# Performance work log

Measured on AMD Instinct MI355X. Metric: run time of the kernel, lower is better.

Reference implementation:

```python
import jax, jax.numpy as jnp
import numpy as np

LMDA = 1.0
SMOOTH = 1e-05

# 13 directional offsets (dz, dy, dx) matching the original slice pairs 1..13
OFFSETS = [
    (1, 0, 0), (0, 1, 0), (0, 0, 1),
    (1, 1, 0), (1, -1, 0),
    (0, 1, 1), (0, 1, -1),
    (1, 0, -1), (1, 0, 1),
    (1, -1, -1), (1, 1, -1),
    (-1, -1, -1), (-1, 1, -1),
]


def _shifted_diff(x, off):
    """x[..., pos-shift] - x[..., neg-shift] for offset off over last 3 dims."""
    sl_pos = tuple(slice(1, None) if o == 1 else (slice(None, -1) if o == -1 else slice(None)) for o in off)
    sl_neg = tuple(slice(None, -1) if o == 1 else (slice(1, None) if o == -1 else slice(None)) for o in off)
    return x[(Ellipsis,) + sl_pos] - x[(Ellipsis,) + sl_neg]


def setup_inputs() -> dict:
    key = jax.random.key(0)
    k1, k2 = jax.random.split(key)
    shape = (4, 1, 128, 192, 192)
    eps = 1e-6
    inp = jax.random.uniform(k1, shape, dtype=jnp.float32, minval=eps, maxval=1.0 - eps)
    tgt = jax.random.uniform(k2, shape, dtype=jnp.float32, minval=0.0, maxval=1.0)
    return {"input": inp, "target": tgt}


def reference(input, target):
    # region term: BCE with mean reduction
    bce = -jnp.mean(target * jnp.log(input) + (1.0 - target) * jnp.log(1.0 - input))

    # boundary term: 13 directional diff-product ratios
    acc = jnp.float32(0.0)
    for off in OFFSETS:
        di = _shifted_diff(input, off)
        dt = _shifted_diff(target, off)
        acc = acc + jnp.sum(di * dt) / (jnp.sum(dt * dt) + SMOOTH)
    boundary = 1.0 - acc / 13.0

    return LMDA * bce + boundary
```

## Files before the change

### kernel.cpp

```cpp
#include <hip/hip_runtime.h>
#include <math.h>

#define DX 192
#define DY 192
#define DZ 128
#define DB 4
#define DXY (DX*DY)
#define NTOT (DB*DZ*DXY)
#define NV (NTOT/4)
#define XV (DX/4)


__device__ inline float wred(float v) {
    #pragma unroll
    for (int o = 32; o > 0; o >>= 1) v += __shfl_down(v, o, 64);
    return v;
}

__global__ __launch_bounds__(256) void gc3d_main(const float* __restrict__ inp,
                                                 const float* __restrict__ tgt,
                                                 double* __restrict__ acc) {
    float s0=0,s1=0,s2=0,s3=0,s4=0,s5=0,s6=0,s7=0,s8=0,s9=0,s10=0,s11=0,s12=0;
    float r0=0,r1=0,r2=0,r3=0,r4=0,r5=0,r6=0,r7=0,r8=0,r9=0,r10=0,r11=0,r12=0;
    float bces = 0.f;

    int tid = blockIdx.x * blockDim.x + threadIdx.x;
    int stride = gridDim.x * blockDim.x;

    for (int v = tid; v < NV; v += stride) {
        int xv4 = v % XV;
        int rem = v / XV;
        int y = rem % DY;
        int z = (rem / DY) % DZ;
        int x0 = xv4 * 4;

        bool zv = (z != DZ - 1);
        bool yv = (y != DY - 1);
        int oz = zv ? DXY : 0;
        int oy = yv ? DX : 0;
        int xe = (x0 != DX - 4) ? 4 : 3;
        float fz = zv ? 1.f : 0.f;
        float fy = yv ? 1.f : 0.f;
        float fx3 = (x0 != DX - 4) ? 1.f : 0.f;

        long base = (long)v * 4;
        const float* ip = inp + base;
        const float* tp = tgt + base;

        float4 i00 = *(const float4*)(ip);
        float4 i01 = *(const float4*)(ip + oy);
        float4 i10 = *(const float4*)(ip + oz);
        float4 i11 = *(const float4*)(ip + oz + oy);
        float4 t00 = *(const float4*)(tp);
        float4 t01 = *(const float4*)(tp + oy);
        float4 t10 = *(const float4*)(tp + oz);
        float4 t11 = *(const float4*)(tp + oz + oy);
        float i00e = ip[xe],        i01e = ip[oy + xe];
        float i10e = ip[oz + xe],   i11e = ip[oz + oy + xe];
        float t00e = tp[xe],        t01e = tp[oy + xe];
        float t10e = tp[oz + xe],   t11e = tp[oz + oy + xe];

        #define PROC_ELEM(c0,c1,c2,c3,c4,c5,c6,c7, d0,d1,d2,d3,d4,d5,d6,d7, FX) do { \
            float fzy = fz*fy, fyx = fy*(FX), fzx = fz*(FX), fzyx = fzy*(FX); \
            float di, dt, dtm; \
            di=c4-c0; dt=d4-d0; dtm=fz  *dt; s0 +=di*dtm; r0 +=dt*dtm; \
            di=c2-c0; dt=d2-d0; dtm=fy  *dt; s1 +=di*dtm; r1 +=dt*dtm; \
            di=c1-c0; dt=d1-d0; dtm=(FX)*dt; s2 +=di*dtm; r2 +=dt*dtm; \
            di=c6-c0; dt=d6-d0; dtm=fzy *dt; s3 +=di*dtm; r3 +=dt*dtm; \
            di=c4-c2; dt=d4-d2; dtm=fzy *dt; s4 +=di*dtm; r4 +=dt*dtm; \
            di=c3-c0; dt=d3-d0; dtm=fyx *dt; s5 +=di*dtm; r5 +=dt*dtm; \
            di=c2-c1; dt=d2-d1; dtm=fyx *dt; s6 +=di*dtm; r6 +=dt*dtm; \
            di=c4-c1; dt=d4-d1; dtm=fzx *dt; s7 +=di*dtm; r7 +=dt*dtm; \
            di=c5-c0; dt=d5-d0; dtm=fzx *dt; s8 +=di*dtm; r8 +=dt*dtm; \
            di=c4-c3; dt=d4-d3; dtm=fzyx*dt; s9 +=di*dtm; r9 +=dt*dtm; \
            di=c6-c1; dt=d6-d1; dtm=fzyx*dt; s10+=di*dtm; r10+=dt*dtm; \
            di=c7-c0; dt=d7-d0; dtm=fzyx*dt; s11+=di*dtm; r11+=dt*dtm; \
            di=c5-c2; dt=d5-d2; dtm=fzyx*dt; s12+=di*dtm; r12+=dt*dtm; \
            bces += d0*__logf(c0) + (1.0f - d0)*__logf(1.0f - c0); \
        } while (0)

        PROC_ELEM(i00.x,i00.y,i01.x,i01.y,i10.x,i10.y,i11.x,i11.y,
                  t00.x,t00.y,t01.x,t01.y,t10.x,t10.y,t11.x,t11.y, 1.0f);
        PROC_ELEM(i00.y,i00.z,i01.y,i01.z,i10.y,i10.z,i11.y,i11.z,
                  t00.y,t00.z,t01.y,t01.z,t10.y,t10.z,t11.y,t11.z, 1.0f);
        PROC_ELEM(i00.z,i00.w,i01.z,i01.w,i10.z,i10.w,i11.z,i11.w,
                  t00.z,t00.w,t01.z,t01.w,t10.z,t10.w,t11.z,t11.w, 1.0f);
        PROC_ELEM(i00.w,i00e, i01.w,i01e, i10.w,i10e, i11.w,i11e,
                  t00.w,t00e, t01.w,t01e, t10.w,t10e, t11.w,t11e, fx3);
        #undef PROC_ELEM
    }

    float vals[27] = {s0,s1,s2,s3,s4,s5,s6,s7,s8,s9,s10,s11,s12,
                      r0,r1,r2,r3,r4,r5,r6,r7,r8,r9,r10,r11,r12, bces};
    #pragma unroll
    for (int k = 0; k < 27; k++) vals[k] = wred(vals[k]);

    __shared__ float red[4][27];
    int lane = threadIdx.x & 63;
    int wave = threadIdx.x >> 6;
    if (lane == 0) {
        #pragma unroll
        for (int k = 0; k < 27; k++) red[wave][k] = vals[k];
    }
    __syncthreads();
    if (threadIdx.x < 27) {
        float t = red[0][threadIdx.x] + red[1][threadIdx.x]
                + red[2][threadIdx.x] + red[3][threadIdx.x];
        atomicAdd(&acc[threadIdx.x], (double)t);
    }
}

__global__ void gc3d_final(const double* __restrict__ acc, float* __restrict__ out) {
    if (threadIdx.x == 0 && blockIdx.x == 0) {
        double s = 0.0;
        #pragma unroll
        for (int k = 0; k < 13; k++) s += acc[k] / (acc[13 + k] + 1e-5);
        double bce = -acc[26] / (double)NTOT;
        out[0] = (float)(bce + 1.0 - s / 13.0);
    }
}

extern "C" void kernel_launch(void* const* d_in, const int* in_sizes, int n_in,
                              void* d_out, int out_size, void* d_ws, size_t ws_size,
                              hipStream_t stream) {
    const float* inp = (const float*)d_in[0];
    const float* tgt = (const float*)d_in[1];
    double* acc = (double*)d_ws;

    hipMemsetAsync(d_ws, 0, 27 * sizeof(double), stream);
    gc3d_main<<<1536, 256, 0, stream>>>(inp, tgt, acc);
    gc3d_final<<<1, 64, 0, stream>>>(acc, (float*)d_out);
}
```

Measured before the change: 224.0 us.

## Tile 8-wide x strips over z-chunks with register reuse and interior specialization

Each thread now handles an 8-element x strip across a 4-slice z chunk, keeping the upper z-plane rows in registers as the next lower plane instead of reloading them. This cuts redundant global and cache loads, since the old version read four rows per four elements. An INTERIOR template drops the boundary mask multiplies for threads away from the z and y edges, and the BCE term is rewritten to use one fewer multiply. The grid is sized exactly to the work, with no grid-stride loop. In exchange each thread holds more registers, there are far more blocks, and each block still issues its own atomics.

```diff
diff --git a/kernel.cpp b/kernel.cpp
--- a/kernel.cpp
+++ b/kernel.cpp
@@ -6,101 +6,133 @@
 #define DZ 128
 #define DB 4
 #define DXY (DX*DY)
-#define NTOT (DB*DZ*DXY)
-#define NV (NTOT/4)
-#define XV (DX/4)
+#define XG 24
+#define ZC 4
+#define NCK (DZ/ZC)
+#define NBLK (DB*NCK*DY*XG/256)
 
 
-__device__ inline float wred(float v) {
+struct Acc { float s[13]; float r[13]; float bce; };
+
+__device__ inline void load9(float (&a)[9], const float* __restrict__ p, int xe) {
+    float4 u = *(const float4*)(p);
+    float4 v = *(const float4*)(p + 4);
+    a[0]=u.x; a[1]=u.y; a[2]=u.z; a[3]=u.w;
+    a[4]=v.x; a[5]=v.y; a[6]=v.z; a[7]=v.w;
+    a[8] = p[xe];
+}
+
+template<bool INTERIOR>
+__device__ inline void compute8(const float (&Ia)[9], const float (&Ib)[9],
+                                const float (&Ja)[9], const float (&Jb)[9],
+                                const float (&Ta)[9], const float (&Tb)[9],
+                                const float (&Ua)[9], const float (&Ub)[9],
+                                float fz, float fy, float fx7, Acc& A)
+{
     #pragma unroll
-    for (int o = 32; o > 0; o >>= 1) v += __shfl_down(v, o, 64);
-    return v;
+    for (int e = 0; e < 8; ++e) {
+        const float fx = (e < 7) ? 1.0f : fx7;
+        float mzy, myx, mzx, mzyx;
+        if (INTERIOR) { mzy = 1.0f; myx = fx; mzx = fx; mzyx = fx; }
+        else { mzy = fz*fy; myx = fy*fx; mzx = fz*fx; mzyx = mzy*fx; }
+        const float c0=Ia[e], c1=Ia[e+1], c2=Ib[e], c3=Ib[e+1];
+        const float c4=Ja[e], c5=Ja[e+1], c6=Jb[e], c7=Jb[e+1];
+        const float d0=Ta[e], d1=Ta[e+1], d2=Tb[e], d3=Tb[e+1];
+        const float d4=Ua[e], d5=Ua[e+1], d6=Ub[e], d7=Ub[e+1];
+        float di, dt, dtm;
+        di=c4-c0; dt=d4-d0;              A.s[0] +=di*dt;  A.r[0] +=dt*dt;
+        di=c2-c0; dt=d2-d0;              A.s[1] +=di*dt;  A.r[1] +=dt*dt;
+        di=c1-c0; dt=d1-d0;              A.s[2] +=di*dt;  A.r[2] +=dt*dt;
+        di=c6-c0; dt=d6-d0; dtm=mzy*dt;  A.s[3] +=di*dtm; A.r[3] +=dt*dtm;
+        di=c4-c2; dt=d4-d2; dtm=mzy*dt;  A.s[4] +=di*dtm; A.r[4] +=dt*dtm;
+        di=c3-c0; dt=d3-d0; dtm=myx*dt;  A.s[5] +=di*dtm; A.r[5] +=dt*dtm;
+        di=c2-c1; dt=d2-d1; dtm=myx*dt;  A.s[6] +=di*dtm; A.r[6] +=dt*dtm;
+        di=c4-c1; dt=d4-d1; dtm=mzx*dt;  A.s[7] +=di*dtm; A.r[7] +=dt*dtm;
+        di=c5-c0; dt=d5-d0; dtm=mzx*dt;  A.s[8] +=di*dtm; A.r[8] +=dt*dtm;
+        di=c4-c3; dt=d4-d3; dtm=mzyx*dt; A.s[9] +=di*dtm; A.r[9] +=dt*dtm;
+        di=c6-c1; dt=d6-d1; dtm=mzyx*dt; A.s[10]+=di*dtm; A.r[10]+=dt*dtm;
+        di=c7-c0; dt=d7-d0; dtm=mzyx*dt; A.s[11]+=di*dtm; A.r[11]+=dt*dtm;
+        di=c5-c2; dt=d5-d2; dtm=mzyx*dt; A.s[12]+=di*dtm; A.r[12]+=dt*dtm;
+        float l0 = __logf(c0), l1 = __logf(1.0f - c0);
+        A.bce += l1 + d0 * (l0 - l1);
+    }
+}
+
+template<bool INTERIOR>
+__device__ inline void zloop(const float* __restrict__ ip, const float* __restrict__ tp,
+                             int oy, int xe, float fy, float fx7, int z0, Acc& A)
+{
+    float Ia[9], Ib[9], Ta[9], Tb[9];
+    float Ja[9], Jb[9], Ua[9], Ub[9];
+    load9(Ia, ip, xe); load9(Ib, ip + oy, xe);
+    load9(Ta, tp, xe); load9(Tb, tp + oy, xe);
+    #pragma unroll 1
+    for (int k = 0; k < ZC/2; ++k) {
+        int z = z0 + 2*k;
+        {
+            int   oz = (INTERIOR || z < DZ-1) ? DXY : 0;
+            float fz = (INTERIOR || z < DZ-1) ? 1.0f : 0.0f;
+            load9(Ja, ip + oz, xe); load9(Jb, ip + oz + oy, xe);
+            load9(Ua, tp + oz, xe); load9(Ub, tp + oz + oy, xe);
+            compute8<INTERIOR>(Ia, Ib, Ja, Jb, Ta, Tb, Ua, Ub, fz, fy, fx7, A);
+            ip += DXY; tp += DXY;
+        }
+        {
+            int z1 = z + 1;
+            int   oz = (INTERIOR || z1 < DZ-1) ? DXY : 0;
+            float fz = (INTERIOR || z1 < DZ-1) ? 1.0f : 0.0f;
+            load9(Ia, ip + oz, xe); load9(Ib, ip + oz + oy, xe);
+            load9(Ta, tp + oz, xe); load9(Tb, tp + oz + oy, xe);
+            compute8<INTERIOR>(Ja, Jb, Ia, Ib, Ua, Ub, Ta, Tb, fz, fy, fx7, A);
+            ip += DXY; tp += DXY;
+        }
+    }
 }
 
 __global__ __launch_bounds__(256) void gc3d_main(const float* __restrict__ inp,
                                                  const float* __restrict__ tgt,
-                                                 double* __restrict__ acc) {
-    float s0=0,s1=0,s2=0,s3=0,s4=0,s5=0,s6=0,s7=0,s8=0,s9=0,s10=0,s11=0,s12=0;
-    float r0=0,r1=0,r2=0,r3=0,r4=0,r5=0,r6=0,r7=0,r8=0,r9=0,r10=0,r11=0,r12=0;
-    float bces = 0.f;
+                                                 double* __restrict__ acc)
+{
+    int gid = blockIdx.x * 256 + threadIdx.x;
+    int xg = gid % XG;
+    int t1 = gid / XG;
+    int y  = t1 % DY;
+    int t2 = t1 / DY;
+    int ck = t2 % NCK;
+    int b  = t2 / NCK;
+    int z0 = ck * ZC;
 
-    int tid = blockIdx.x * blockDim.x + threadIdx.x;
-    int stride = gridDim.x * blockDim.x;
+    long base = (((long)b * DZ + z0) * DY + y) * DX + xg * 8;
+    const float* ip = inp + base;
+    const float* tp = tgt + base;
+    int   oy  = (y < DY-1) ? DX : 0;
+    float fy  = (y < DY-1) ? 1.0f : 0.0f;
+    int   xe  = (xg < XG-1) ? 8 : 7;
+    float fx7 = (xg < XG-1) ? 1.0f : 0.0f;
 
-    for (int v = tid; v < NV; v += stride) {
-        int xv4 = v % XV;
-        int rem = v / XV;
-        int y = rem % DY;
-        int z = (rem / DY) % DZ;
-        int x0 = xv4 * 4;
+    Acc A;
+    #pragma unroll
+    for (int k = 0; k < 13; ++k) { A.s[k] = 0.f; A.r[k] = 0.f; }
+    A.bce = 0.f;
 
-        bool zv = (z != DZ - 1);
-        bool yv = (y != DY - 1);
-        int oz = zv ? DXY : 0;
-        int oy = yv ? DX : 0;
-        int xe = (x0 != DX - 4) ? 4 : 3;
-        float fz = zv ? 1.f : 0.f;
-        float fy = yv ? 1.f : 0.f;
-        float fx3 = (x0 != DX - 4) ? 1.f : 0.f;
+    if ((y < DY-1) && (ck < NCK-1)) zloop<true >(ip, tp, oy, xe, fy, fx7, z0, A);
+    else                            zloop<false>(ip, tp, oy, xe, fy, fx7, z0, A);
 
-        long base = (long)v * 4;
-        const float* ip = inp + base;
-        const float* tp = tgt + base;
-
-        float4 i00 = *(const float4*)(ip);
-        float4 i01 = *(const float4*)(ip + oy);
-        float4 i10 = *(const float4*)(ip + oz);
-        float4 i11 = *(const float4*)(ip + oz + oy);
-        float4 t00 = *(const float4*)(tp);
-        float4 t01 = *(const float4*)(tp + oy);
-        float4 t10 = *(const float4*)(tp + oz);
-        float4 t11 = *(const float4*)(tp + oz + oy);
-        float i00e = ip[xe],        i01e = ip[oy + xe];
-        float i10e = ip[oz + xe],   i11e = ip[oz + oy + xe];
-        float t00e = tp[xe],        t01e = tp[oy + xe];
-        float t10e = tp[oz + xe],   t11e = tp[oz + oy + xe];
-
-        #define PROC_ELEM(c0,c1,c2,c3,c4,c5,c6,c7, d0,d1,d2,d3,d4,d5,d6,d7, FX) do { \
-            float fzy = fz*fy, fyx = fy*(FX), fzx = fz*(FX), fzyx = fzy*(FX); \
-            float di, dt, dtm; \
-            di=c4-c0; dt=d4-d0; dtm=fz  *dt; s0 +=di*dtm; r0 +=dt*dtm; \
-            di=c2-c0; dt=d2-d0; dtm=fy  *dt; s1 +=di*dtm; r1 +=dt*dtm; \
-            di=c1-c0; dt=d1-d0; dtm=(FX)*dt; s2 +=di*dtm; r2 +=dt*dtm; \
-            di=c6-c0; dt=d6-d0; dtm=fzy *dt; s3 +=di*dtm; r3 +=dt*dtm; \
-            di=c4-c2; dt=d4-d2; dtm=fzy *dt; s4 +=di*dtm; r4 +=dt*dtm; \
-            di=c3-c0; dt=d3-d0; dtm=fyx *dt; s5 +=di*dtm; r5 +=dt*dtm; \
-            di=c2-c1; dt=d2-d1; dtm=fyx *dt; s6 +=di*dtm; r6 +=dt*dtm; \
-            di=c4-c1; dt=d4-d1; dtm=fzx *dt; s7 +=di*dtm; r7 +=dt*dtm; \
-            di=c5-c0; dt=d5-d0; dtm=fzx *dt; s8 +=di*dtm; r8 +=dt*dtm; \
-            di=c4-c3; dt=d4-d3; dtm=fzyx*dt; s9 +=di*dtm; r9 +=dt*dtm; \
-            di=c6-c1; dt=d6-d1; dtm=fzyx*dt; s10+=di*dtm; r10+=dt*dtm; \
-            di=c7-c0; dt=d7-d0; dtm=fzyx*dt; s11+=di*dtm; r11+=dt*dtm; \
-            di=c5-c2; dt=d5-d2; dtm=fzyx*dt; s12+=di*dtm; r12+=dt*dtm; \
-            bces += d0*__logf(c0) + (1.0f - d0)*__logf(1.0f - c0); \
-        } while (0)
-
-        PROC_ELEM(i00.x,i00.y,i01.x,i01.y,i10.x,i10.y,i11.x,i11.y,
-                  t00.x,t00.y,t01.x,t01.y,t10.x,t10.y,t11.x,t11.y, 1.0f);
-        PROC_ELEM(i00.y,i00.z,i01.y,i01.z,i10.y,i10.z,i11.y,i11.z,
-                  t00.y,t00.z,t01.y,t01.z,t10.y,t10.z,t11.y,t11.z, 1.0f);
-        PROC_ELEM(i00.z,i00.w,i01.z,i01.w,i10.z,i10.w,i11.z,i11.w,
-                  t00.z,t00.w,t01.z,t01.w,t10.z,t10.w,t11.z,t11.w, 1.0f);
-        PROC_ELEM(i00.w,i00e, i01.w,i01e, i10.w,i10e, i11.w,i11e,
-                  t00.w,t00e, t01.w,t01e, t10.w,t10e, t11.w,t11e, fx3);
-        #undef PROC_ELEM
+    float vals[27];
+    #pragma unroll
+    for (int k = 0; k < 13; ++k) { vals[k] = A.s[k]; vals[13+k] = A.r[k]; }
+    vals[26] = A.bce;
+    #pragma unroll
+    for (int k = 0; k < 27; ++k) {
+        #pragma unroll
+        for (int o = 32; o > 0; o >>= 1) vals[k] += __shfl_down(vals[k], o, 64);
     }
-
-    float vals[27] = {s0,s1,s2,s3,s4,s5,s6,s7,s8,s9,s10,s11,s12,
-                      r0,r1,r2,r3,r4,r5,r6,r7,r8,r9,r10,r11,r12, bces};
-    #pragma unroll
-    for (int k = 0; k < 27; k++) vals[k] = wred(vals[k]);
-
     __shared__ float red[4][27];
     int lane = threadIdx.x & 63;
     int wave = threadIdx.x >> 6;
     if (lane == 0) {
         #pragma unroll
-        for (int k = 0; k < 27; k++) red[wave][k] = vals[k];
+        for (int k = 0; k < 27; ++k) red[wave][k] = vals[k];
     }
     __syncthreads();
     if (threadIdx.x < 27) {
@@ -114,8 +146,8 @@
     if (threadIdx.x == 0 && blockIdx.x == 0) {
         double s = 0.0;
         #pragma unroll
-        for (int k = 0; k < 13; k++) s += acc[k] / (acc[13 + k] + 1e-5);
-        double bce = -acc[26] / (double)NTOT;
+        for (int k = 0; k < 13; ++k) s += acc[k] / (acc[13 + k] + 1e-5);
+        double bce = -acc[26] / (double)((long)DB * DZ * DY * DX);
         out[0] = (float)(bce + 1.0 - s / 13.0);
     }
 }
@@ -128,6 +160,6 @@
     double* acc = (double*)d_ws;
 
     hipMemsetAsync(d_ws, 0, 27 * sizeof(double), stream);
-    gc3d_main<<<1536, 256, 0, stream>>>(inp, tgt, acc);
+    gc3d_main<<<NBLK, 256, 0, stream>>>(inp, tgt, acc);
     gc3d_final<<<1, 64, 0, stream>>>(acc, (float*)d_out);
 }
```

Result: slower. 291.1 us (+29.9%).

## Use packed float2 math and shifted unaligned float4 loads for neighbor stencil

Applied to the files above, without the earlier changes.

Rewrites the per-element stencil to work on two-wide float vectors so the compiler can emit packed FP32 instructions, halving the scalar ALU op count. The 4 scalar edge loads per stream are replaced by unaligned float4 loads shifted by one element, giving the x+1 neighbors directly. It also switches to unsigned index math, drops the always-one z and y masks on the pure-z and pure-y directions, and simplifies the BCE expression to one multiply. The unaligned loads may split across cache lines and double the vector load instructions, and the bound guard on the shifted load adds index logic.

```diff
diff --git a/kernel.cpp b/kernel.cpp
--- a/kernel.cpp
+++ b/kernel.cpp
@@ -6,101 +6,121 @@
 #define DZ 128
 #define DB 4
 #define DXY (DX*DY)
-#define NTOT (DB*DZ*DXY)
-#define NV (NTOT/4)
+#define NTOT ((long)DB*DZ*DY*DX)
+#define NV ((unsigned)(NTOT/4))
 #define XV (DX/4)
+#define NBLK 1536
 
 
-__device__ inline float wred(float v) {
-    #pragma unroll
-    for (int o = 32; o > 0; o >>= 1) v += __shfl_down(v, o, 64);
-    return v;
+typedef float v2f __attribute__((ext_vector_type(2)));
+
+struct __attribute__((packed, aligned(4))) f4u { float x, y, z, w; };
+
+__device__ __forceinline__ float4 ld4 (const float* p){ return *(const float4*)p; }
+__device__ __forceinline__ float4 ld4u(const float* p){
+    f4u t = *(const f4u*)p;
+    float4 r; r.x=t.x; r.y=t.y; r.z=t.z; r.w=t.w; return r;
+}
+__device__ __forceinline__ v2f lo(float4 a){ v2f r = {a.x, a.y}; return r; }
+__device__ __forceinline__ v2f hi(float4 a){ v2f r = {a.z, a.w}; return r; }
+__device__ __forceinline__ v2f spl(float s){ v2f r = {s, s}; return r; }
+
+__device__ __forceinline__ void core(
+    v2f c0,v2f c1,v2f c2,v2f c3,v2f c4,v2f c5,v2f c6,v2f c7,
+    v2f d0,v2f d1,v2f d2,v2f d3,v2f d4,v2f d5,v2f d6,v2f d7,
+    v2f mx, v2f mzy, v2f myx, v2f mzx, v2f mzyx, v2f (&A)[27])
+{
+    v2f di, dt, dtm;
+    di=c4-c0; dt=d4-d0;              A[0] +=di*dt;  A[13]+=dt*dt;
+    di=c2-c0; dt=d2-d0;              A[1] +=di*dt;  A[14]+=dt*dt;
+    di=c1-c0; dt=d1-d0; dtm=mx*dt;   A[2] +=di*dtm; A[15]+=dt*dtm;
+    di=c6-c0; dt=d6-d0; dtm=mzy*dt;  A[3] +=di*dtm; A[16]+=dt*dtm;
+    di=c4-c2; dt=d4-d2; dtm=mzy*dt;  A[4] +=di*dtm; A[17]+=dt*dtm;
+    di=c3-c0; dt=d3-d0; dtm=myx*dt;  A[5] +=di*dtm; A[18]+=dt*dtm;
+    di=c2-c1; dt=d2-d1; dtm=myx*dt;  A[6] +=di*dtm; A[19]+=dt*dtm;
+    di=c4-c1; dt=d4-d1; dtm=mzx*dt;  A[7] +=di*dtm; A[20]+=dt*dtm;
+    di=c5-c0; dt=d5-d0; dtm=mzx*dt;  A[8] +=di*dtm; A[21]+=dt*dtm;
+    di=c4-c3; dt=d4-d3; dtm=mzyx*dt; A[9] +=di*dtm; A[22]+=dt*dtm;
+    di=c6-c1; dt=d6-d1; dtm=mzyx*dt; A[10]+=di*dtm; A[23]+=dt*dtm;
+    di=c7-c0; dt=d7-d0; dtm=mzyx*dt; A[11]+=di*dtm; A[24]+=dt*dtm;
+    di=c5-c2; dt=d5-d2; dtm=mzyx*dt; A[12]+=di*dtm; A[25]+=dt*dtm;
 }
 
 __global__ __launch_bounds__(256) void gc3d_main(const float* __restrict__ inp,
                                                  const float* __restrict__ tgt,
-                                                 double* __restrict__ acc) {
-    float s0=0,s1=0,s2=0,s3=0,s4=0,s5=0,s6=0,s7=0,s8=0,s9=0,s10=0,s11=0,s12=0;
-    float r0=0,r1=0,r2=0,r3=0,r4=0,r5=0,r6=0,r7=0,r8=0,r9=0,r10=0,r11=0,r12=0;
-    float bces = 0.f;
+                                                 double* __restrict__ acc)
+{
+    v2f A[27];
+    #pragma unroll
+    for (int k = 0; k < 27; ++k) A[k] = spl(0.f);
 
-    int tid = blockIdx.x * blockDim.x + threadIdx.x;
-    int stride = gridDim.x * blockDim.x;
+    unsigned tid = blockIdx.x * 256 + threadIdx.x;
+    const unsigned stride = NBLK * 256;
 
-    for (int v = tid; v < NV; v += stride) {
-        int xv4 = v % XV;
-        int rem = v / XV;
-        int y = rem % DY;
-        int z = (rem / DY) % DZ;
-        int x0 = xv4 * 4;
+    #pragma unroll 1
+    for (unsigned v = tid; v < NV; v += stride) {
+        unsigned xv4 = v % XV;
+        unsigned rem = v / XV;
+        unsigned y   = rem % DY;
+        unsigned z   = (rem / DY) & (DZ - 1);
 
-        bool zv = (z != DZ - 1);
-        bool yv = (y != DY - 1);
-        int oz = zv ? DXY : 0;
-        int oy = yv ? DX : 0;
-        int xe = (x0 != DX - 4) ? 4 : 3;
-        float fz = zv ? 1.f : 0.f;
-        float fy = yv ? 1.f : 0.f;
-        float fx3 = (x0 != DX - 4) ? 1.f : 0.f;
-
-        long base = (long)v * 4;
+        size_t base = (size_t)v * 4;
         const float* ip = inp + base;
         const float* tp = tgt + base;
+        int   oy  = (y < DY-1) ? DX  : 0;
+        int   oz  = (z < DZ-1) ? DXY : 0;
+        float fy  = (y < DY-1) ? 1.f : 0.f;
+        float fz  = (z < DZ-1) ? 1.f : 0.f;
+        float fx3 = (xv4 < XV-1) ? 1.f : 0.f;
+        int   xo  = (base + (size_t)oz + (size_t)oy + 8 <= (size_t)NTOT) ? 1 : 0;
+        float fzy = fz * fy;
 
-        float4 i00 = *(const float4*)(ip);
-        float4 i01 = *(const float4*)(ip + oy);
-        float4 i10 = *(const float4*)(ip + oz);
-        float4 i11 = *(const float4*)(ip + oz + oy);
-        float4 t00 = *(const float4*)(tp);
-        float4 t01 = *(const float4*)(tp + oy);
-        float4 t10 = *(const float4*)(tp + oz);
-        float4 t11 = *(const float4*)(tp + oz + oy);
-        float i00e = ip[xe],        i01e = ip[oy + xe];
-        float i10e = ip[oz + xe],   i11e = ip[oz + oy + xe];
-        float t00e = tp[xe],        t01e = tp[oy + xe];
-        float t10e = tp[oz + xe],   t11e = tp[oz + oy + xe];
+        float4 i00=ld4(ip),        i00x=ld4u(ip+xo);
+        float4 i01=ld4(ip+oy),     i01x=ld4u(ip+oy+xo);
+        float4 i10=ld4(ip+oz),     i10x=ld4u(ip+oz+xo);
+        float4 i11=ld4(ip+oz+oy),  i11x=ld4u(ip+oz+oy+xo);
+        float4 t00=ld4(tp),        t00x=ld4u(tp+xo);
+        float4 t01=ld4(tp+oy),     t01x=ld4u(tp+oy+xo);
+        float4 t10=ld4(tp+oz),     t10x=ld4u(tp+oz+xo);
+        float4 t11=ld4(tp+oz+oy),  t11x=ld4u(tp+oz+oy+xo);
 
-        #define PROC_ELEM(c0,c1,c2,c3,c4,c5,c6,c7, d0,d1,d2,d3,d4,d5,d6,d7, FX) do { \
-            float fzy = fz*fy, fyx = fy*(FX), fzx = fz*(FX), fzyx = fzy*(FX); \
-            float di, dt, dtm; \
-            di=c4-c0; dt=d4-d0; dtm=fz  *dt; s0 +=di*dtm; r0 +=dt*dtm; \
-            di=c2-c0; dt=d2-d0; dtm=fy  *dt; s1 +=di*dtm; r1 +=dt*dtm; \
-            di=c1-c0; dt=d1-d0; dtm=(FX)*dt; s2 +=di*dtm; r2 +=dt*dtm; \
-            di=c6-c0; dt=d6-d0; dtm=fzy *dt; s3 +=di*dtm; r3 +=dt*dtm; \
-            di=c4-c2; dt=d4-d2; dtm=fzy *dt; s4 +=di*dtm; r4 +=dt*dtm; \
-            di=c3-c0; dt=d3-d0; dtm=fyx *dt; s5 +=di*dtm; r5 +=dt*dtm; \
-            di=c2-c1; dt=d2-d1; dtm=fyx *dt; s6 +=di*dtm; r6 +=dt*dtm; \
-            di=c4-c1; dt=d4-d1; dtm=fzx *dt; s7 +=di*dtm; r7 +=dt*dtm; \
-            di=c5-c0; dt=d5-d0; dtm=fzx *dt; s8 +=di*dtm; r8 +=dt*dtm; \
-            di=c4-c3; dt=d4-d3; dtm=fzyx*dt; s9 +=di*dtm; r9 +=dt*dtm; \
-            di=c6-c1; dt=d6-d1; dtm=fzyx*dt; s10+=di*dtm; r10+=dt*dtm; \
-            di=c7-c0; dt=d7-d0; dtm=fzyx*dt; s11+=di*dtm; r11+=dt*dtm; \
-            di=c5-c2; dt=d5-d2; dtm=fzyx*dt; s12+=di*dtm; r12+=dt*dtm; \
-            bces += d0*__logf(c0) + (1.0f - d0)*__logf(1.0f - c0); \
-        } while (0)
-
-        PROC_ELEM(i00.x,i00.y,i01.x,i01.y,i10.x,i10.y,i11.x,i11.y,
-                  t00.x,t00.y,t01.x,t01.y,t10.x,t10.y,t11.x,t11.y, 1.0f);
-        PROC_ELEM(i00.y,i00.z,i01.y,i01.z,i10.y,i10.z,i11.y,i11.z,
-                  t00.y,t00.z,t01.y,t01.z,t10.y,t10.z,t11.y,t11.z, 1.0f);
-        PROC_ELEM(i00.z,i00.w,i01.z,i01.w,i10.z,i10.w,i11.z,i11.w,
-                  t00.z,t00.w,t01.z,t01.w,t10.z,t10.w,t11.z,t11.w, 1.0f);
-        PROC_ELEM(i00.w,i00e, i01.w,i01e, i10.w,i10e, i11.w,i11e,
-                  t00.w,t00e, t01.w,t01e, t10.w,t10e, t11.w,t11e, fx3);
-        #undef PROC_ELEM
+        {
+            v2f one = {1.f, 1.f};
+            core(lo(i00),lo(i00x),lo(i01),lo(i01x),lo(i10),lo(i10x),lo(i11),lo(i11x),
+                 lo(t00),lo(t00x),lo(t01),lo(t01x),lo(t10),lo(t10x),lo(t11),lo(t11x),
+                 one, spl(fzy), spl(fy), spl(fz), spl(fzy), A);
+            v2f p = lo(i00), q = lo(t00);
+            v2f l0 = { __logf(p.x),       __logf(p.y)       };
+            v2f l1 = { __logf(1.f - p.x), __logf(1.f - p.y) };
+            A[26] += l1 + q * (l0 - l1);
+        }
+        {
+            v2f fxv = {1.f, fx3};
+            core(hi(i00),hi(i00x),hi(i01),hi(i01x),hi(i10),hi(i10x),hi(i11),hi(i11x),
+                 hi(t00),hi(t00x),hi(t01),hi(t01x),hi(t10),hi(t10x),hi(t11),hi(t11x),
+                 fxv, spl(fzy), fxv*fy, fxv*fz, fxv*fzy, A);
+            v2f p = hi(i00), q = hi(t00);
+            v2f l0 = { __logf(p.x),       __logf(p.y)       };
+            v2f l1 = { __logf(1.f - p.x), __logf(1.f - p.y) };
+            A[26] += l1 + q * (l0 - l1);
+        }
     }
 
-    float vals[27] = {s0,s1,s2,s3,s4,s5,s6,s7,s8,s9,s10,s11,s12,
-                      r0,r1,r2,r3,r4,r5,r6,r7,r8,r9,r10,r11,r12, bces};
+    float vals[27];
     #pragma unroll
-    for (int k = 0; k < 27; k++) vals[k] = wred(vals[k]);
+    for (int k = 0; k < 27; ++k) vals[k] = A[k].x + A[k].y;
+    #pragma unroll
+    for (int k = 0; k < 27; ++k) {
+        #pragma unroll
+        for (int o = 32; o > 0; o >>= 1) vals[k] += __shfl_down(vals[k], o, 64);
+    }
 
     __shared__ float red[4][27];
     int lane = threadIdx.x & 63;
     int wave = threadIdx.x >> 6;
     if (lane == 0) {
         #pragma unroll
-        for (int k = 0; k < 27; k++) red[wave][k] = vals[k];
+        for (int k = 0; k < 27; ++k) red[wave][k] = vals[k];
     }
     __syncthreads();
     if (threadIdx.x < 27) {
@@ -114,7 +134,7 @@
     if (threadIdx.x == 0 && blockIdx.x == 0) {
         double s = 0.0;
         #pragma unroll
-        for (int k = 0; k < 13; k++) s += acc[k] / (acc[13 + k] + 1e-5);
+        for (int k = 0; k < 13; ++k) s += acc[k] / (acc[13 + k] + 1e-5);
         double bce = -acc[26] / (double)NTOT;
         out[0] = (float)(bce + 1.0 - s / 13.0);
     }
@@ -128,6 +148,6 @@
     double* acc = (double*)d_ws;
 
     hipMemsetAsync(d_ws, 0, 27 * sizeof(double), stream);
-    gc3d_main<<<1536, 256, 0, stream>>>(inp, tgt, acc);
+    gc3d_main<<<NBLK, 256, 0, stream>>>(inp, tgt, acc);
     gc3d_final<<<1, 64, 0, stream>>>(acc, (float*)d_out);
 }
```

Result: no change. 226.2 us (+1.0%).
